# Optimization experiments

Measured on AMD Instinct MI355X. Metric: run time of the kernel, lower is better.

The kernel has to match this reference:

```python
import jax, jax.numpy as jnp
import numpy as np

DIM = 192
HEADS = 6
WIN = 64  # 8*8
EPS = 1e-12


def setup_inputs() -> dict:
    key = jax.random.key(0)
    ks = jax.random.split(key, 10)
    s = 0.02
    return {
        "qx": jax.random.normal(ks[0], (8192, WIN, DIM), jnp.float32),
        "kvx": jax.random.normal(ks[1], (4096, WIN, DIM), jnp.float32),
        "pos": jax.random.normal(ks[2], (1, WIN, DIM), jnp.float32) * s,
        "Wq": jax.random.normal(ks[3], (DIM, DIM), jnp.float32) * s,
        "bq": jnp.zeros((DIM,), jnp.float32),
        "Wkv": jax.random.normal(ks[4], (2 * DIM, DIM), jnp.float32) * s,
        "bkv": jnp.zeros((2 * DIM,), jnp.float32),
        "Wp": jax.random.normal(ks[5], (DIM, DIM), jnp.float32) * s,
        "bp": jnp.zeros((DIM,), jnp.float32),
    }


def _l2norm(x):
    # F.normalize: x / max(||x||_2, eps) along last dim
    n = jnp.sqrt(jnp.sum(x * x, axis=-1, keepdims=True))
    return x / jnp.maximum(n, EPS)


def reference(qx, kvx, pos, Wq, bq, Wkv, bkv, Wp, bp):
    B_q, q_len, C = qx.shape
    B_kv, kv_len, _ = kvx.shape
    tile_num = B_q // B_kv
    kvx = jnp.tile(kvx, (tile_num, 1, 1))
    qx = qx + pos
    q = qx @ Wq.T + bq                       # [Bq, q, C]
    kv = kvx @ Wkv.T + bkv                   # [Bq, kv, 2C]
    k, v = kv[..., :C], kv[..., C:]
    hd = C // HEADS
    q = q.reshape(B_q, q_len, HEADS, hd).transpose(0, 2, 1, 3)
    k = k.reshape(B_q, kv_len, HEADS, hd).transpose(0, 2, 1, 3)
    v = v.reshape(B_q, kv_len, HEADS, hd).transpose(0, 2, 1, 3)
    scale = 1.0 / np.sqrt(C).astype(np.float32)
    attn = jnp.einsum("bhqd,bhkd->bhqk", _l2norm(q), _l2norm(k)) * scale
    attn = jax.nn.softmax(attn, axis=-1)
    x = jnp.einsum("bhqk,bhkd->bhqd", attn, v)
    x = x.transpose(0, 2, 1, 3).reshape(B_q, q_len, C)
    return x @ Wp.T + bp
```

## Files before the change

kernel.cpp:

```cpp
#include <hip/hip_runtime.h>
#include <hip/hip_bf16.h>

#define TPB   512
#define CDIM  192
#define LDA   200
#define LDK   200
#define LDVT  72
#define LDST  200
#define VTOFF 12800
#define SCALE 0.07216878364870323f
#define EPSF  1e-12f

using short8 = __attribute__((ext_vector_type(8))) short;
using f32x4  = __attribute__((ext_vector_type(4))) float;
using us4    = __attribute__((ext_vector_type(4))) unsigned short;

__device__ __forceinline__ unsigned short hc(float f) {
  __hip_bfloat16 h = __float2bfloat16(f);
  unsigned short u; __builtin_memcpy(&u, &h, 2); return u;
}
__device__ __forceinline__ unsigned pack2(float x, float y) {
  return (unsigned)hc(x) | ((unsigned)hc(y) << 16);
}
__device__ __forceinline__ uint2 packa(f32x4 a) {
  return make_uint2(pack2(a[0], a[1]), pack2(a[2], a[3]));
}
#define MFMA(a, b, c) __builtin_amdgcn_mfma_f32_16x16x32_bf16((a), (b), (c), 0, 0, 0)
#define SCHED_FENCE() __builtin_amdgcn_sched_barrier(0)

#define NWQ  36864
#define NWKV 73728
#define NWP  36864
__global__ void cvt_weights(const float* __restrict__ Wq, const float* __restrict__ Wkv,
                            const float* __restrict__ Wp, unsigned short* __restrict__ o) {
  int i = blockIdx.x * blockDim.x + threadIdx.x;
  if (i < NWQ) o[i] = hc(Wq[i]);
  else if (i < NWQ + NWKV) o[i] = hc(Wkv[i - NWQ]);
  else if (i < NWQ + NWKV + NWP) o[i] = hc(Wp[i - NWQ - NWKV]);
}

__global__ __launch_bounds__(TPB, 4) void wa_v16(
    const float* __restrict__ qx, const float* __restrict__ kvx,
    const float* __restrict__ pos,
    const float* __restrict__ bq, const float* __restrict__ bkv,
    const float* __restrict__ bp,
    const unsigned short* __restrict__ Wqb, const unsigned short* __restrict__ Wkvb,
    const unsigned short* __restrict__ Wpb,
    float* __restrict__ out, int BQ, int BKV)
{
  __shared__ __align__(16) unsigned short sA[64 * LDA];
  __shared__ __align__(16) unsigned short sU[26624];

  const int tid = threadIdx.x;
  const int wid = tid >> 6;
  const int l15 = (tid & 63) & 15;
  const int l4  = (tid & 63) >> 4;

  int g = blockIdx.x;
  int w;
  if (BQ == 2 * BKV && (BKV & 7) == 0) {
    w = ((g >> 4) << 3) + (g & 7) + (((g >> 3) & 1) ? BKV : 0);
  } else {
    w = g;
  }
  const size_t qoff  = (size_t)w * (64 * CDIM);
  const size_t kvoff = (size_t)(w % BKV) * (64 * CDIM);

  const int srcA = l15 + 32 * (l4 & 1);
  const int srcB = srcA + 16;
  const int sel  = l4 >> 1;
  auto redistC = [&](f32x4 cA, f32x4 cB) -> short8 {
    unsigned iA0 = pack2(cA[0], cA[1]), iA1 = pack2(cA[2], cA[3]);
    unsigned iB0 = pack2(cB[0], cB[1]), iB1 = pack2(cB[2], cB[3]);
    unsigned A00 = (unsigned)__shfl((int)iA0, srcA);
    unsigned A01 = (unsigned)__shfl((int)iA1, srcA);
    unsigned A10 = (unsigned)__shfl((int)iB0, srcA);
    unsigned A11 = (unsigned)__shfl((int)iB1, srcA);
    unsigned B00 = (unsigned)__shfl((int)iA0, srcB);
    unsigned B01 = (unsigned)__shfl((int)iA1, srcB);
    unsigned B10 = (unsigned)__shfl((int)iB0, srcB);
    unsigned B11 = (unsigned)__shfl((int)iB1, srcB);
    union { uint4 u; short8 s; } uu;
    uu.u.x = sel ? A10 : A00;
    uu.u.y = sel ? A11 : A01;
    uu.u.z = sel ? B10 : B00;
    uu.u.w = sel ? B11 : B01;
    return uu.s;
  };

  {
    const float4* gq = (const float4*)(qx + qoff);
    const float4* p4 = (const float4*)pos;
    #pragma unroll
    for (int t = 0; t < 6; ++t) {
      int e = tid + t * TPB, row = e / 48, c4 = e % 48;
      float4 a = gq[e], p = p4[e];
      us4 wq;
      wq.x = hc(a.x + p.x); wq.y = hc(a.y + p.y); wq.z = hc(a.z + p.z); wq.w = hc(a.w + p.w);
      *(us4*)&sA[row * LDA + c4 * 4] = wq;
    }
    const float4* gk = (const float4*)(kvx + kvoff);
    #pragma unroll
    for (int t = 0; t < 6; ++t) {
      int e = tid + t * TPB, row = e / 48, c4 = e % 48;
      float4 k = gk[e];
      us4 wk; wk.x = hc(k.x); wk.y = hc(k.y); wk.z = hc(k.z); wk.w = hc(k.w);
      *(us4*)&sU[row * LDST + c4 * 4] = wk;
    }
  }
  __syncthreads();

  auto kproj = [&](int h, short8* kres) {
    f32x4 kacc[4][2];
    #pragma unroll
    for (int mh = 0; mh < 2; ++mh) {
      float4 bk = *(const float4*)&bkv[32 * h + 16 * mh + 4 * l4];
      #pragma unroll
      for (int n = 0; n < 4; ++n) kacc[n][mh] = f32x4{bk.x, bk.y, bk.z, bk.w};
    }
    #pragma unroll
    for (int ks = 0; ks < 6; ++ks) {
      short8 act[4];
      #pragma unroll
      for (int n = 0; n < 4; ++n)
        act[n] = *(const short8*)&sU[(16 * n + l15) * LDST + ks * 32 + 8 * l4];
      #pragma unroll
      for (int mh = 0; mh < 2; ++mh) {
        short8 kw = *(const short8*)&Wkvb[(size_t)(32 * h + 16 * mh + l15) * CDIM + ks * 32 + 8 * l4];
        #pragma unroll
        for (int n = 0; n < 4; ++n) kacc[n][mh] = MFMA(kw, act[n], kacc[n][mh]);
      }
    }
    #pragma unroll
    for (int n = 0; n < 4; ++n) {
      float ss = 0.f;
      #pragma unroll
      for (int mh = 0; mh < 2; ++mh)
        #pragma unroll
        for (int r = 0; r < 4; ++r) ss += kacc[n][mh][r] * kacc[n][mh][r];
      ss += __shfl_xor(ss, 16);
      ss += __shfl_xor(ss, 32);
      float sc = 1.0f / fmaxf(sqrtf(ss), EPSF);
      #pragma unroll
      for (int mh = 0; mh < 2; ++mh)
        #pragma unroll
        for (int r = 0; r < 4; ++r) kacc[n][mh][r] *= sc;
      kres[n] = redistC(kacc[n][0], kacc[n][1]);
    }
  };
  auto vhalf = [&](int h, int nv) {
    f32x4 vacc[4];
    {
      float bv = bkv[CDIM + 32 * h + 16 * nv + l15];
      #pragma unroll
      for (int m = 0; m < 4; ++m) vacc[m] = f32x4{bv, bv, bv, bv};
    }
    #pragma unroll
    for (int ks = 0; ks < 6; ++ks) {
      short8 vw = *(const short8*)&Wkvb[(size_t)(CDIM + 32 * h + 16 * nv + l15) * CDIM + ks * 32 + 8 * l4];
      #pragma unroll
      for (int m = 0; m < 4; ++m) {
        short8 act = *(const short8*)&sU[(16 * m + l15) * LDST + ks * 32 + 8 * l4];
        vacc[m] = MFMA(act, vw, vacc[m]);
      }
    }
    #pragma unroll
    for (int m = 0; m < 4; ++m)
      *(uint2*)&sU[VTOFF + (32 * h + 16 * nv + l15) * LDVT + 16 * m + 4 * l4] = packa(vacc[m]);
  };
  auto qproj = [&](int h, short8* qres) {
    f32x4 qacc[4][2];
    #pragma unroll
    for (int mh = 0; mh < 2; ++mh) {
      float4 bk = *(const float4*)&bq[32 * h + 16 * mh + 4 * l4];
      #pragma unroll
      for (int n = 0; n < 4; ++n) qacc[n][mh] = f32x4{bk.x, bk.y, bk.z, bk.w};
    }
    #pragma unroll
    for (int ks = 0; ks < 6; ++ks) {
      short8 act[4];
      #pragma unroll
      for (int n = 0; n < 4; ++n)
        act[n] = *(const short8*)&sA[(16 * n + l15) * LDA + ks * 32 + 8 * l4];
      #pragma unroll
      for (int mh = 0; mh < 2; ++mh) {
        short8 qw = *(const short8*)&Wqb[(size_t)(32 * h + 16 * mh + l15) * CDIM + ks * 32 + 8 * l4];
        #pragma unroll
        for (int n = 0; n < 4; ++n) qacc[n][mh] = MFMA(qw, act[n], qacc[n][mh]);
      }
    }
    #pragma unroll
    for (int n = 0; n < 4; ++n) {
      float ss = 0.f;
      #pragma unroll
      for (int mh = 0; mh < 2; ++mh)
        #pragma unroll
        for (int r = 0; r < 4; ++r) ss += qacc[n][mh][r] * qacc[n][mh][r];
      ss += __shfl_xor(ss, 16);
      ss += __shfl_xor(ss, 32);
      float sc = SCALE / fmaxf(sqrtf(ss), EPSF);
      #pragma unroll
      for (int mh = 0; mh < 2; ++mh)
        #pragma unroll
        for (int r = 0; r < 4; ++r) qacc[n][mh][r] *= sc;
      qres[n] = redistC(qacc[n][0], qacc[n][1]);
    }
  };

  short8 kres[4];
  const bool hasK = (wid < 6);
  if (hasK) {
    kproj(wid, kres);
    SCHED_FENCE();
    vhalf(wid >> 1, wid & 1);
  } else {
    const int t0 = 6 + (wid - 6) * 3;
    vhalf(t0 >> 1, t0 & 1);
    SCHED_FENCE();
    vhalf((t0 + 1) >> 1, (t0 + 1) & 1);
    SCHED_FENCE();
    vhalf((t0 + 2) >> 1, (t0 + 2) & 1);
  }
  __syncthreads();

  if (hasK) {
    #pragma unroll
    for (int n = 0; n < 4; ++n)
      *(short8*)&sU[(16 * n + l15) * LDK + wid * 32 + 8 * l4] = kres[n];
  }
  SCHED_FENCE();
  short8 qres[4];
  if (wid < 6) qproj(wid, qres);
  __syncthreads();

  if (wid < 6) {
    #pragma unroll
    for (int n = 0; n < 4; ++n)
      *(short8*)&sA[(16 * n + l15) * LDA + wid * 32 + 8 * l4] = qres[n];
  }
  __syncthreads();

  {
    const int t  = wid & 3;
    const int h0 = 3 * (wid >> 2);
    #pragma unroll
    for (int i = 0; i < 3; ++i) {
      const int hh = h0 + i;
      short8 qb = *(const short8*)&sA[(16 * t + l15) * LDA + hh * 32 + 8 * l4];
      f32x4 c[4];
      #pragma unroll
      for (int n = 0; n < 4; ++n) {
        short8 ak = *(const short8*)&sU[(16 * n + l15) * LDK + hh * 32 + 8 * l4];
        f32x4 z = f32x4{0.f, 0.f, 0.f, 0.f};
        c[n] = MFMA(ak, qb, z);
      }
      float sum = 0.f;
      #pragma unroll
      for (int n = 0; n < 4; ++n)
        #pragma unroll
        for (int r = 0; r < 4; ++r) { c[n][r] = __expf(c[n][r]); sum += c[n][r]; }
      sum += __shfl_xor(sum, 16);
      sum += __shfl_xor(sum, 32);
      const float inv = 1.0f / sum;
      #pragma unroll
      for (int n = 0; n < 4; ++n)
        #pragma unroll
        for (int r = 0; r < 4; ++r) c[n][r] *= inv;
      short8 pa0 = redistC(c[0], c[1]);
      short8 pa1 = redistC(c[2], c[3]);
      f32x4 cx0 = f32x4{0.f, 0.f, 0.f, 0.f};
      f32x4 cx1 = f32x4{0.f, 0.f, 0.f, 0.f};
      {
        short8 av00 = *(const short8*)&sU[VTOFF + (hh * 32 + l15) * LDVT + 8 * l4];
        short8 av01 = *(const short8*)&sU[VTOFF + (hh * 32 + l15) * LDVT + 32 + 8 * l4];
        cx0 = MFMA(av00, pa0, cx0);
        cx0 = MFMA(av01, pa1, cx0);
        short8 av10 = *(const short8*)&sU[VTOFF + (hh * 32 + 16 + l15) * LDVT + 8 * l4];
        short8 av11 = *(const short8*)&sU[VTOFF + (hh * 32 + 16 + l15) * LDVT + 32 + 8 * l4];
        cx1 = MFMA(av10, pa0, cx1);
        cx1 = MFMA(av11, pa1, cx1);
      }
      short8 xf = redistC(cx0, cx1);
      *(short8*)&sA[(16 * t + l15) * LDA + hh * 32 + 8 * l4] = xf;
    }
  }
  __syncthreads();

  {
    {
      const int n = wid;
      f32x4 oacc[4];
      float bv = bp[n * 16 + l15];
      #pragma unroll
      for (int m = 0; m < 4; ++m) oacc[m] = f32x4{bv, bv, bv, bv};
      #pragma unroll
      for (int ks = 0; ks < 6; ++ks) {
        short8 pw = *(const short8*)&Wpb[(size_t)(n * 16 + l15) * CDIM + ks * 32 + 8 * l4];
        #pragma unroll
        for (int m = 0; m < 4; ++m) {
          short8 xa = *(const short8*)&sA[(16 * m + l15) * LDA + ks * 32 + 8 * l4];
          oacc[m] = MFMA(xa, pw, oacc[m]);
        }
      }
      #pragma unroll
      for (int m = 0; m < 4; ++m)
        #pragma unroll
        for (int r = 0; r < 4; ++r)
          out[qoff + (size_t)(16 * m + 4 * l4 + r) * CDIM + n * 16 + l15] = oacc[m][r];
    }
    SCHED_FENCE();
    if (wid < 4) {
      const int n = wid + 8;
      f32x4 oacc[4];
      float bv = bp[n * 16 + l15];
      #pragma unroll
      for (int m = 0; m < 4; ++m) oacc[m] = f32x4{bv, bv, bv, bv};
      #pragma unroll
      for (int ks = 0; ks < 6; ++ks) {
        short8 pw = *(const short8*)&Wpb[(size_t)(n * 16 + l15) * CDIM + ks * 32 + 8 * l4];
        #pragma unroll
        for (int m = 0; m < 4; ++m) {
          short8 xa = *(const short8*)&sA[(16 * m + l15) * LDA + ks * 32 + 8 * l4];
          oacc[m] = MFMA(xa, pw, oacc[m]);
        }
      }
      #pragma unroll
      for (int m = 0; m < 4; ++m)
        #pragma unroll
        for (int r = 0; r < 4; ++r)
          out[qoff + (size_t)(16 * m + 4 * l4 + r) * CDIM + n * 16 + l15] = oacc[m][r];
    }
  }
}

extern "C" void kernel_launch(void* const* d_in, const int* in_sizes, int n_in,
                              void* d_out, int out_size, void* d_ws, size_t ws_size,
                              hipStream_t stream) {
  const float* qx  = (const float*)d_in[0];
  const float* kvx = (const float*)d_in[1];
  const float* pos = (const float*)d_in[2];
  const float* Wq  = (const float*)d_in[3];
  const float* bq  = (const float*)d_in[4];
  const float* Wkv = (const float*)d_in[5];
  const float* bkv = (const float*)d_in[6];
  const float* Wp  = (const float*)d_in[7];
  const float* bp  = (const float*)d_in[8];
  float* out = (float*)d_out;
  unsigned short* wsb = (unsigned short*)d_ws;

  const int BQ  = in_sizes[0] / (64 * CDIM);
  const int BKV = in_sizes[1] / (64 * CDIM);

  const int ncvt = NWQ + NWKV + NWP;
  cvt_weights<<<(ncvt + 255) / 256, 256, 0, stream>>>(Wq, Wkv, Wp, wsb);

  wa_v16<<<BQ, TPB, 0, stream>>>(qx, kvx, pos, bq, bkv, bp,
                                 wsb, wsb + NWQ, wsb + NWQ + NWKV, out, BQ, BKV);
}
```

Measured before the change: 465.8 us.

## Fuse output projection into attention waves with split-K reduction via LDS

Each wave now keeps its attention output fragments in registers and immediately multiplies them by the Wp slice for its three heads, accumulating all 12 output column tiles. The two wave groups that cover different head halves are then reduced through shared memory before storing. This removes the write of attention output to LDS and the separate full projection pass, but holds 12 accumulators per wave, which raises register pressure. The L2-norm and softmax divisions are also replaced with hardware rsq/rcp intrinsics.

```diff
diff --git a/kernel.cpp b/kernel.cpp
--- a/kernel.cpp
+++ b/kernel.cpp
@@ -9,7 +9,6 @@
 #define LDST  200
 #define VTOFF 12800
 #define SCALE 0.07216878364870323f
-#define EPSF  1e-12f
 
 using short8 = __attribute__((ext_vector_type(8))) short;
 using f32x4  = __attribute__((ext_vector_type(4))) float;
@@ -39,7 +38,7 @@
   else if (i < NWQ + NWKV + NWP) o[i] = hc(Wp[i - NWQ - NWKV]);
 }
 
-__global__ __launch_bounds__(TPB, 4) void wa_v16(
+__global__ __launch_bounds__(TPB, 4) void wa_v17(
     const float* __restrict__ qx, const float* __restrict__ kvx,
     const float* __restrict__ pos,
     const float* __restrict__ bq, const float* __restrict__ bkv,
@@ -140,7 +139,7 @@
         for (int r = 0; r < 4; ++r) ss += kacc[n][mh][r] * kacc[n][mh][r];
       ss += __shfl_xor(ss, 16);
       ss += __shfl_xor(ss, 32);
-      float sc = 1.0f / fmaxf(sqrtf(ss), EPSF);
+      float sc = __builtin_amdgcn_rsqf(fmaxf(ss, 1e-24f));
       #pragma unroll
       for (int mh = 0; mh < 2; ++mh)
         #pragma unroll
@@ -198,7 +197,7 @@
         for (int r = 0; r < 4; ++r) ss += qacc[n][mh][r] * qacc[n][mh][r];
       ss += __shfl_xor(ss, 16);
       ss += __shfl_xor(ss, 32);
-      float sc = SCALE / fmaxf(sqrtf(ss), EPSF);
+      float sc = SCALE * __builtin_amdgcn_rsqf(fmaxf(ss, 1e-24f));
       #pragma unroll
       for (int mh = 0; mh < 2; ++mh)
         #pragma unroll
@@ -240,9 +239,12 @@
   }
   __syncthreads();
 
+  const int t  = wid & 3;
+  const int tr = wid >> 2;
+  const int h0 = 3 * tr;
+  f32x4 oacc[12];
   {
-    const int t  = wid & 3;
-    const int h0 = 3 * (wid >> 2);
+    short8 xa[3];
     #pragma unroll
     for (int i = 0; i < 3; ++i) {
       const int hh = h0 + i;
@@ -261,7 +263,7 @@
         for (int r = 0; r < 4; ++r) { c[n][r] = __expf(c[n][r]); sum += c[n][r]; }
       sum += __shfl_xor(sum, 16);
       sum += __shfl_xor(sum, 32);
-      const float inv = 1.0f / sum;
+      const float inv = __builtin_amdgcn_rcpf(sum);
       #pragma unroll
       for (int n = 0; n < 4; ++n)
         #pragma unroll
@@ -280,55 +282,41 @@
         cx1 = MFMA(av10, pa0, cx1);
         cx1 = MFMA(av11, pa1, cx1);
       }
-      short8 xf = redistC(cx0, cx1);
-      *(short8*)&sA[(16 * t + l15) * LDA + hh * 32 + 8 * l4] = xf;
-    }
+      xa[i] = redistC(cx0, cx1);
+    }
+    SCHED_FENCE();
+    #pragma unroll
+    for (int n = 0; n < 12; ++n) {
+      float bv = (tr == 0) ? bp[n * 16 + l15] : 0.f;
+      oacc[n] = f32x4{bv, bv, bv, bv};
+    }
+    #pragma unroll
+    for (int i = 0; i < 3; ++i)
+      #pragma unroll
+      for (int n = 0; n < 12; ++n) {
+        short8 pw = *(const short8*)&Wpb[(size_t)(n * 16 + l15) * CDIM + (h0 + i) * 32 + 8 * l4];
+        oacc[n] = MFMA(xa[i], pw, oacc[n]);
+      }
   }
   __syncthreads();
 
   {
-    {
-      const int n = wid;
-      f32x4 oacc[4];
-      float bv = bp[n * 16 + l15];
-      #pragma unroll
-      for (int m = 0; m < 4; ++m) oacc[m] = f32x4{bv, bv, bv, bv};
-      #pragma unroll
-      for (int ks = 0; ks < 6; ++ks) {
-        short8 pw = *(const short8*)&Wpb[(size_t)(n * 16 + l15) * CDIM + ks * 32 + 8 * l4];
-        #pragma unroll
-        for (int m = 0; m < 4; ++m) {
-          short8 xa = *(const short8*)&sA[(16 * m + l15) * LDA + ks * 32 + 8 * l4];
-          oacc[m] = MFMA(xa, pw, oacc[m]);
-        }
-      }
-      #pragma unroll
-      for (int m = 0; m < 4; ++m)
+    float* pool = (t < 2) ? (float*)sA + t * 3072 : (float*)sU + (t - 2) * 3072;
+    const int lane = tid & 63;
+    if (tr == 1) {
+      #pragma unroll
+      for (int n = 0; n < 12; ++n)
+        *(f32x4*)(pool + n * 256 + lane * 4) = oacc[n];
+    }
+    __syncthreads();
+    if (tr == 0) {
+      #pragma unroll
+      for (int n = 0; n < 12; ++n) {
+        f32x4 p = *(const f32x4*)(pool + n * 256 + lane * 4);
         #pragma unroll
         for (int r = 0; r < 4; ++r)
-          out[qoff + (size_t)(16 * m + 4 * l4 + r) * CDIM + n * 16 + l15] = oacc[m][r];
-    }
-    SCHED_FENCE();
-    if (wid < 4) {
-      const int n = wid + 8;
-      f32x4 oacc[4];
-      float bv = bp[n * 16 + l15];
-      #pragma unroll
-      for (int m = 0; m < 4; ++m) oacc[m] = f32x4{bv, bv, bv, bv};
-      #pragma unroll
-      for (int ks = 0; ks < 6; ++ks) {
-        short8 pw = *(const short8*)&Wpb[(size_t)(n * 16 + l15) * CDIM + ks * 32 + 8 * l4];
-        #pragma unroll
-        for (int m = 0; m < 4; ++m) {
-          short8 xa = *(const short8*)&sA[(16 * m + l15) * LDA + ks * 32 + 8 * l4];
-          oacc[m] = MFMA(xa, pw, oacc[m]);
-        }
-      }
-      #pragma unroll
-      for (int m = 0; m < 4; ++m)
-        #pragma unroll
-        for (int r = 0; r < 4; ++r)
-          out[qoff + (size_t)(16 * m + 4 * l4 + r) * CDIM + n * 16 + l15] = oacc[m][r];
+          out[qoff + (size_t)(16 * t + 4 * l4 + r) * CDIM + n * 16 + l15] = oacc[n][r] + p[r];
+      }
     }
   }
 }
@@ -354,6 +342,6 @@
   const int ncvt = NWQ + NWKV + NWP;
   cvt_weights<<<(ncvt + 255) / 256, 256, 0, stream>>>(Wq, Wkv, Wp, wsb);
 
-  wa_v16<<<BQ, TPB, 0, stream>>>(qx, kvx, pos, bq, bkv, bp,
+  wa_v17<<<BQ, TPB, 0, stream>>>(qx, kvx, pos, bq, bkv, bp,
                                  wsb, wsb + NWQ, wsb + NWQ + NWKV, out, BQ, BKV);
 }
```

Result: slower. 614.4 us (+31.9%).

## Compute K/V projection once per kv window and loop over tiled query windows

Applied to the files above, without the earlier changes.

The launch now uses one block per kv window instead of one per query window. Each block projects and normalises K and V once, then loops over the tile_num query windows that share that kv window, running Q projection, attention and output projection for each. This removes the duplicated K/V projection and the duplicate kvx loads. In exchange the grid is halved (4096 blocks) and each block's work is serialised, with extra barriers around each query pass.

```diff
diff --git a/kernel.cpp b/kernel.cpp
--- a/kernel.cpp
+++ b/kernel.cpp
@@ -39,14 +39,14 @@
   else if (i < NWQ + NWKV + NWP) o[i] = hc(Wp[i - NWQ - NWKV]);
 }
 
-__global__ __launch_bounds__(TPB, 4) void wa_v16(
+__global__ __launch_bounds__(TPB, 4) void wa_v18(
     const float* __restrict__ qx, const float* __restrict__ kvx,
     const float* __restrict__ pos,
     const float* __restrict__ bq, const float* __restrict__ bkv,
     const float* __restrict__ bp,
     const unsigned short* __restrict__ Wqb, const unsigned short* __restrict__ Wkvb,
     const unsigned short* __restrict__ Wpb,
-    float* __restrict__ out, int BQ, int BKV)
+    float* __restrict__ out, int BKV, int tile_num)
 {
   __shared__ __align__(16) unsigned short sA[64 * LDA];
   __shared__ __align__(16) unsigned short sU[26624];
@@ -55,16 +55,7 @@
   const int wid = tid >> 6;
   const int l15 = (tid & 63) & 15;
   const int l4  = (tid & 63) >> 4;
-
-  int g = blockIdx.x;
-  int w;
-  if (BQ == 2 * BKV && (BKV & 7) == 0) {
-    w = ((g >> 4) << 3) + (g & 7) + (((g >> 3) & 1) ? BKV : 0);
-  } else {
-    w = g;
-  }
-  const size_t qoff  = (size_t)w * (64 * CDIM);
-  const size_t kvoff = (size_t)(w % BKV) * (64 * CDIM);
+  const size_t kvoff = (size_t)blockIdx.x * (64 * CDIM);
 
   const int srcA = l15 + 32 * (l4 & 1);
   const int srcB = srcA + 16;
@@ -88,8 +79,8 @@
     return uu.s;
   };
 
-  {
-    const float4* gq = (const float4*)(qx + qoff);
+  auto stage_q = [&](size_t qo) {
+    const float4* gq = (const float4*)(qx + qo);
     const float4* p4 = (const float4*)pos;
     #pragma unroll
     for (int t = 0; t < 6; ++t) {
@@ -99,6 +90,211 @@
       wq.x = hc(a.x + p.x); wq.y = hc(a.y + p.y); wq.z = hc(a.z + p.z); wq.w = hc(a.w + p.w);
       *(us4*)&sA[row * LDA + c4 * 4] = wq;
     }
+  };
+
+  auto kproj = [&](int h, short8* kres) {
+    f32x4 kacc[4][2];
+    #pragma unroll
+    for (int mh = 0; mh < 2; ++mh) {
+      float4 bk = *(const float4*)&bkv[32 * h + 16 * mh + 4 * l4];
+      #pragma unroll
+      for (int n = 0; n < 4; ++n) kacc[n][mh] = f32x4{bk.x, bk.y, bk.z, bk.w};
+    }
+    #pragma unroll
+    for (int ks = 0; ks < 6; ++ks) {
+      short8 act[4];
+      #pragma unroll
+      for (int n = 0; n < 4; ++n)
+        act[n] = *(const short8*)&sU[(16 * n + l15) * LDST + ks * 32 + 8 * l4];
+      #pragma unroll
+      for (int mh = 0; mh < 2; ++mh) {
+        short8 kw = *(const short8*)&Wkvb[(size_t)(32 * h + 16 * mh + l15) * CDIM + ks * 32 + 8 * l4];
+        #pragma unroll
+        for (int n = 0; n < 4; ++n) kacc[n][mh] = MFMA(kw, act[n], kacc[n][mh]);
+      }
+    }
+    #pragma unroll
+    for (int n = 0; n < 4; ++n) {
+      float ss = 0.f;
+      #pragma unroll
+      for (int mh = 0; mh < 2; ++mh)
+        #pragma unroll
+        for (int r = 0; r < 4; ++r) ss += kacc[n][mh][r] * kacc[n][mh][r];
+      ss += __shfl_xor(ss, 16);
+      ss += __shfl_xor(ss, 32);
+      float sc = 1.0f / fmaxf(sqrtf(ss), EPSF);
+      #pragma unroll
+      for (int mh = 0; mh < 2; ++mh)
+        #pragma unroll
+        for (int r = 0; r < 4; ++r) kacc[n][mh][r] *= sc;
+      kres[n] = redistC(kacc[n][0], kacc[n][1]);
+    }
+  };
+  auto vhalf = [&](int h, int nv) {
+    f32x4 vacc[4];
+    {
+      float bv = bkv[CDIM + 32 * h + 16 * nv + l15];
+      #pragma unroll
+      for (int m = 0; m < 4; ++m) vacc[m] = f32x4{bv, bv, bv, bv};
+    }
+    #pragma unroll
+    for (int ks = 0; ks < 6; ++ks) {
+      short8 vw = *(const short8*)&Wkvb[(size_t)(CDIM + 32 * h + 16 * nv + l15) * CDIM + ks * 32 + 8 * l4];
+      #pragma unroll
+      for (int m = 0; m < 4; ++m) {
+        short8 act = *(const short8*)&sU[(16 * m + l15) * LDST + ks * 32 + 8 * l4];
+        vacc[m] = MFMA(act, vw, vacc[m]);
+      }
+    }
+    #pragma unroll
+    for (int m = 0; m < 4; ++m)
+      *(uint2*)&sU[VTOFF + (32 * h + 16 * nv + l15) * LDVT + 16 * m + 4 * l4] = packa(vacc[m]);
+  };
+  auto qproj = [&](int h, short8* qres) {
+    f32x4 qacc[4][2];
+    #pragma unroll
+    for (int mh = 0; mh < 2; ++mh) {
+      float4 bk = *(const float4*)&bq[32 * h + 16 * mh + 4 * l4];
+      #pragma unroll
+      for (int n = 0; n < 4; ++n) qacc[n][mh] = f32x4{bk.x, bk.y, bk.z, bk.w};
+    }
+    #pragma unroll
+    for (int ks = 0; ks < 6; ++ks) {
+      short8 act[4];
+      #pragma unroll
+      for (int n = 0; n < 4; ++n)
+        act[n] = *(const short8*)&sA[(16 * n + l15) * LDA + ks * 32 + 8 * l4];
+      #pragma unroll
+      for (int mh = 0; mh < 2; ++mh) {
+        short8 qw = *(const short8*)&Wqb[(size_t)(32 * h + 16 * mh + l15) * CDIM + ks * 32 + 8 * l4];
+        #pragma unroll
+        for (int n = 0; n < 4; ++n) qacc[n][mh] = MFMA(qw, act[n], qacc[n][mh]);
+      }
+    }
+    #pragma unroll
+    for (int n = 0; n < 4; ++n) {
+      float ss = 0.f;
+      #pragma unroll
+      for (int mh = 0; mh < 2; ++mh)
+        #pragma unroll
+        for (int r = 0; r < 4; ++r) ss += qacc[n][mh][r] * qacc[n][mh][r];
+      ss += __shfl_xor(ss, 16);
+      ss += __shfl_xor(ss, 32);
+      float sc = SCALE / fmaxf(sqrtf(ss), EPSF);
+      #pragma unroll
+      for (int mh = 0; mh < 2; ++mh)
+        #pragma unroll
+        for (int r = 0; r < 4; ++r) qacc[n][mh][r] *= sc;
+      qres[n] = redistC(qacc[n][0], qacc[n][1]);
+    }
+  };
+
+  auto window_pass = [&](size_t qoff) {
+    short8 qres[4];
+    if (wid < 6) qproj(wid, qres);
+    __syncthreads();
+    if (wid < 6) {
+      #pragma unroll
+      for (int n = 0; n < 4; ++n)
+        *(short8*)&sA[(16 * n + l15) * LDA + wid * 32 + 8 * l4] = qres[n];
+    }
+    __syncthreads();
+
+    {
+      const int t  = wid & 3;
+      const int h0 = 3 * (wid >> 2);
+      #pragma unroll
+      for (int i = 0; i < 3; ++i) {
+        const int hh = h0 + i;
+        short8 qb = *(const short8*)&sA[(16 * t + l15) * LDA + hh * 32 + 8 * l4];
+        f32x4 c[4];
+        #pragma unroll
+        for (int n = 0; n < 4; ++n) {
+          short8 ak = *(const short8*)&sU[(16 * n + l15) * LDK + hh * 32 + 8 * l4];
+          f32x4 z = f32x4{0.f, 0.f, 0.f, 0.f};
+          c[n] = MFMA(ak, qb, z);
+        }
+        float sum = 0.f;
+        #pragma unroll
+        for (int n = 0; n < 4; ++n)
+          #pragma unroll
+          for (int r = 0; r < 4; ++r) { c[n][r] = __expf(c[n][r]); sum += c[n][r]; }
+        sum += __shfl_xor(sum, 16);
+        sum += __shfl_xor(sum, 32);
+        const float inv = 1.0f / sum;
+        #pragma unroll
+        for (int n = 0; n < 4; ++n)
+          #pragma unroll
+          for (int r = 0; r < 4; ++r) c[n][r] *= inv;
+        short8 pa0 = redistC(c[0], c[1]);
+        short8 pa1 = redistC(c[2], c[3]);
+        f32x4 cx0 = f32x4{0.f, 0.f, 0.f, 0.f};
+        f32x4 cx1 = f32x4{0.f, 0.f, 0.f, 0.f};
+        {
+          short8 av00 = *(const short8*)&sU[VTOFF + (hh * 32 + l15) * LDVT + 8 * l4];
+          short8 av01 = *(const short8*)&sU[VTOFF + (hh * 32 + l15) * LDVT + 32 + 8 * l4];
+          cx0 = MFMA(av00, pa0, cx0);
+          cx0 = MFMA(av01, pa1, cx0);
+          short8 av10 = *(const short8*)&sU[VTOFF + (hh * 32 + 16 + l15) * LDVT + 8 * l4];
+          short8 av11 = *(const short8*)&sU[VTOFF + (hh * 32 + 16 + l15) * LDVT + 32 + 8 * l4];
+          cx1 = MFMA(av10, pa0, cx1);
+          cx1 = MFMA(av11, pa1, cx1);
+        }
+        short8 xf = redistC(cx0, cx1);
+        *(short8*)&sA[(16 * t + l15) * LDA + hh * 32 + 8 * l4] = xf;
+      }
+    }
+    __syncthreads();
+
+    {
+      {
+        const int n = wid;
+        f32x4 oacc[4];
+        float bv = bp[n * 16 + l15];
+        #pragma unroll
+        for (int m = 0; m < 4; ++m) oacc[m] = f32x4{bv, bv, bv, bv};
+        #pragma unroll
+        for (int ks = 0; ks < 6; ++ks) {
+          short8 pw = *(const short8*)&Wpb[(size_t)(n * 16 + l15) * CDIM + ks * 32 + 8 * l4];
+          #pragma unroll
+          for (int m = 0; m < 4; ++m) {
+            short8 xa = *(const short8*)&sA[(16 * m + l15) * LDA + ks * 32 + 8 * l4];
+            oacc[m] = MFMA(xa, pw, oacc[m]);
+          }
+        }
+        #pragma unroll
+        for (int m = 0; m < 4; ++m)
+          #pragma unroll
+          for (int r = 0; r < 4; ++r)
+            out[qoff + (size_t)(16 * m + 4 * l4 + r) * CDIM + n * 16 + l15] = oacc[m][r];
+      }
+      SCHED_FENCE();
+      if (wid < 4) {
+        const int n = wid + 8;
+        f32x4 oacc[4];
+        float bv = bp[n * 16 + l15];
+        #pragma unroll
+        for (int m = 0; m < 4; ++m) oacc[m] = f32x4{bv, bv, bv, bv};
+        #pragma unroll
+        for (int ks = 0; ks < 6; ++ks) {
+          short8 pw = *(const short8*)&Wpb[(size_t)(n * 16 + l15) * CDIM + ks * 32 + 8 * l4];
+          #pragma unroll
+          for (int m = 0; m < 4; ++m) {
+            short8 xa = *(const short8*)&sA[(16 * m + l15) * LDA + ks * 32 + 8 * l4];
+            oacc[m] = MFMA(xa, pw, oacc[m]);
+          }
+        }
+        #pragma unroll
+        for (int m = 0; m < 4; ++m)
+          #pragma unroll
+          for (int r = 0; r < 4; ++r)
+            out[qoff + (size_t)(16 * m + 4 * l4 + r) * CDIM + n * 16 + l15] = oacc[m][r];
+      }
+    }
+  };
+
+  stage_q(kvoff);
+  {
     const float4* gk = (const float4*)(kvx + kvoff);
     #pragma unroll
     for (int t = 0; t < 6; ++t) {
@@ -109,103 +305,6 @@
     }
   }
   __syncthreads();
-
-  auto kproj = [&](int h, short8* kres) {
-    f32x4 kacc[4][2];
-    #pragma unroll
-    for (int mh = 0; mh < 2; ++mh) {
-      float4 bk = *(const float4*)&bkv[32 * h + 16 * mh + 4 * l4];
-      #pragma unroll
-      for (int n = 0; n < 4; ++n) kacc[n][mh] = f32x4{bk.x, bk.y, bk.z, bk.w};
-    }
-    #pragma unroll
-    for (int ks = 0; ks < 6; ++ks) {
-      short8 act[4];
-      #pragma unroll
-      for (int n = 0; n < 4; ++n)
-        act[n] = *(const short8*)&sU[(16 * n + l15) * LDST + ks * 32 + 8 * l4];
-      #pragma unroll
-      for (int mh = 0; mh < 2; ++mh) {
-        short8 kw = *(const short8*)&Wkvb[(size_t)(32 * h + 16 * mh + l15) * CDIM + ks * 32 + 8 * l4];
-        #pragma unroll
-        for (int n = 0; n < 4; ++n) kacc[n][mh] = MFMA(kw, act[n], kacc[n][mh]);
-      }
-    }
-    #pragma unroll
-    for (int n = 0; n < 4; ++n) {
-      float ss = 0.f;
-      #pragma unroll
-      for (int mh = 0; mh < 2; ++mh)
-        #pragma unroll
-        for (int r = 0; r < 4; ++r) ss += kacc[n][mh][r] * kacc[n][mh][r];
-      ss += __shfl_xor(ss, 16);
-      ss += __shfl_xor(ss, 32);
-      float sc = 1.0f / fmaxf(sqrtf(ss), EPSF);
-      #pragma unroll
-      for (int mh = 0; mh < 2; ++mh)
-        #pragma unroll
-        for (int r = 0; r < 4; ++r) kacc[n][mh][r] *= sc;
-      kres[n] = redistC(kacc[n][0], kacc[n][1]);
-    }
-  };
-  auto vhalf = [&](int h, int nv) {
-    f32x4 vacc[4];
-    {
-      float bv = bkv[CDIM + 32 * h + 16 * nv + l15];
-      #pragma unroll
-      for (int m = 0; m < 4; ++m) vacc[m] = f32x4{bv, bv, bv, bv};
-    }
-    #pragma unroll
-    for (int ks = 0; ks < 6; ++ks) {
-      short8 vw = *(const short8*)&Wkvb[(size_t)(CDIM + 32 * h + 16 * nv + l15) * CDIM + ks * 32 + 8 * l4];
-      #pragma unroll
-      for (int m = 0; m < 4; ++m) {
-        short8 act = *(const short8*)&sU[(16 * m + l15) * LDST + ks * 32 + 8 * l4];
-        vacc[m] = MFMA(act, vw, vacc[m]);
-      }
-    }
-    #pragma unroll
-    for (int m = 0; m < 4; ++m)
-      *(uint2*)&sU[VTOFF + (32 * h + 16 * nv + l15) * LDVT + 16 * m + 4 * l4] = packa(vacc[m]);
-  };
-  auto qproj = [&](int h, short8* qres) {
-    f32x4 qacc[4][2];
-    #pragma unroll
-    for (int mh = 0; mh < 2; ++mh) {
-      float4 bk = *(const float4*)&bq[32 * h + 16 * mh + 4 * l4];
-      #pragma unroll
-      for (int n = 0; n < 4; ++n) qacc[n][mh] = f32x4{bk.x, bk.y, bk.z, bk.w};
-    }
-    #pragma unroll
-    for (int ks = 0; ks < 6; ++ks) {
-      short8 act[4];
-      #pragma unroll
-      for (int n = 0; n < 4; ++n)
-        act[n] = *(const short8*)&sA[(16 * n + l15) * LDA + ks * 32 + 8 * l4];
-      #pragma unroll
-      for (int mh = 0; mh < 2; ++mh) {
-        short8 qw = *(const short8*)&Wqb[(size_t)(32 * h + 16 * mh + l15) * CDIM + ks * 32 + 8 * l4];
-        #pragma unroll
-        for (int n = 0; n < 4; ++n) qacc[n][mh] = MFMA(qw, act[n], qacc[n][mh]);
-      }
-    }
-    #pragma unroll
-    for (int n = 0; n < 4; ++n) {
-      float ss = 0.f;
-      #pragma unroll
-      for (int mh = 0; mh < 2; ++mh)
-        #pragma unroll
-        for (int r = 0; r < 4; ++r) ss += qacc[n][mh][r] * qacc[n][mh][r];
-      ss += __shfl_xor(ss, 16);
-      ss += __shfl_xor(ss, 32);
-      float sc = SCALE / fmaxf(sqrtf(ss), EPSF);
-      #pragma unroll
-      for (int mh = 0; mh < 2; ++mh)
-        #pragma unroll
-        for (int r = 0; r < 4; ++r) qacc[n][mh][r] *= sc;
-      qres[n] = redistC(qacc[n][0], qacc[n][1]);
-    }
-  };
 
   short8 kres[4];
   const bool hasK = (wid < 6);
@@ -229,107 +328,14 @@
       *(short8*)&sU[(16 * n + l15) * LDK + wid * 32 + 8 * l4] = kres[n];
   }
   SCHED_FENCE();
-  short8 qres[4];
-  if (wid < 6) qproj(wid, qres);
-  __syncthreads();
-
-  if (wid < 6) {
-    #pragma unroll
-    for (int n = 0; n < 4; ++n)
-      *(short8*)&sA[(16 * n + l15) * LDA + wid * 32 + 8 * l4] = qres[n];
-  }
-  __syncthreads();
-
-  {
-    const int t  = wid & 3;
-    const int h0 = 3 * (wid >> 2);
-    #pragma unroll
-    for (int i = 0; i < 3; ++i) {
-      const int hh = h0 + i;
-      short8 qb = *(const short8*)&sA[(16 * t + l15) * LDA + hh * 32 + 8 * l4];
-      f32x4 c[4];
-      #pragma unroll
-      for (int n = 0; n < 4; ++n) {
-        short8 ak = *(const short8*)&sU[(16 * n + l15) * LDK + hh * 32 + 8 * l4];
-        f32x4 z = f32x4{0.f, 0.f, 0.f, 0.f};
-        c[n] = MFMA(ak, qb, z);
-      }
-      float sum = 0.f;
-      #pragma unroll
-      for (int n = 0; n < 4; ++n)
-        #pragma unroll
-        for (int r = 0; r < 4; ++r) { c[n][r] = __expf(c[n][r]); sum += c[n][r]; }
-      sum += __shfl_xor(sum, 16);
-      sum += __shfl_xor(sum, 32);
-      const float inv = 1.0f / sum;
-      #pragma unroll
-      for (int n = 0; n < 4; ++n)
-        #pragma unroll
-        for (int r = 0; r < 4; ++r) c[n][r] *= inv;
-      short8 pa0 = redistC(c[0], c[1]);
-      short8 pa1 = redistC(c[2], c[3]);
-      f32x4 cx0 = f32x4{0.f, 0.f, 0.f, 0.f};
-      f32x4 cx1 = f32x4{0.f, 0.f, 0.f, 0.f};
-      {
-        short8 av00 = *(const short8*)&sU[VTOFF + (hh * 32 + l15) * LDVT + 8 * l4];
-        short8 av01 = *(const short8*)&sU[VTOFF + (hh * 32 + l15) * LDVT + 32 + 8 * l4];
-        cx0 = MFMA(av00, pa0, cx0);
-        cx0 = MFMA(av01, pa1, cx0);
-        short8 av10 = *(const short8*)&sU[VTOFF + (hh * 32 + 16 + l15) * LDVT + 8 * l4];
-        short8 av11 = *(const short8*)&sU[VTOFF + (hh * 32 + 16 + l15) * LDVT + 32 + 8 * l4];
-        cx1 = MFMA(av10, pa0, cx1);
-        cx1 = MFMA(av11, pa1, cx1);
-      }
-      short8 xf = redistC(cx0, cx1);
-      *(short8*)&sA[(16 * t + l15) * LDA + hh * 32 + 8 * l4] = xf;
-    }
-  }
-  __syncthreads();
-
-  {
-    {
-      const int n = wid;
-      f32x4 oacc[4];
-      float bv = bp[n * 16 + l15];
-      #pragma unroll
-      for (int m = 0; m < 4; ++m) oacc[m] = f32x4{bv, bv, bv, bv};
-      #pragma unroll
-      for (int ks = 0; ks < 6; ++ks) {
-        short8 pw = *(const short8*)&Wpb[(size_t)(n * 16 + l15) * CDIM + ks * 32 + 8 * l4];
-        #pragma unroll
-        for (int m = 0; m < 4; ++m) {
-          short8 xa = *(const short8*)&sA[(16 * m + l15) * LDA + ks * 32 + 8 * l4];
-          oacc[m] = MFMA(xa, pw, oacc[m]);
-        }
-      }
-      #pragma unroll
-      for (int m = 0; m < 4; ++m)
-        #pragma unroll
-        for (int r = 0; r < 4; ++r)
-          out[qoff + (size_t)(16 * m + 4 * l4 + r) * CDIM + n * 16 + l15] = oacc[m][r];
-    }
-    SCHED_FENCE();
-    if (wid < 4) {
-      const int n = wid + 8;
-      f32x4 oacc[4];
-      float bv = bp[n * 16 + l15];
-      #pragma unroll
-      for (int m = 0; m < 4; ++m) oacc[m] = f32x4{bv, bv, bv, bv};
-      #pragma unroll
-      for (int ks = 0; ks < 6; ++ks) {
-        short8 pw = *(const short8*)&Wpb[(size_t)(n * 16 + l15) * CDIM + ks * 32 + 8 * l4];
-        #pragma unroll
-        for (int m = 0; m < 4; ++m) {
-          short8 xa = *(const short8*)&sA[(16 * m + l15) * LDA + ks * 32 + 8 * l4];
-          oacc[m] = MFMA(xa, pw, oacc[m]);
-        }
-      }
-      #pragma unroll
-      for (int m = 0; m < 4; ++m)
-        #pragma unroll
-        for (int r = 0; r < 4; ++r)
-          out[qoff + (size_t)(16 * m + 4 * l4 + r) * CDIM + n * 16 + l15] = oacc[m][r];
-    }
+  window_pass(kvoff);
+
+  for (int j = 1; j < tile_num; ++j) {
+    __syncthreads();
+    const size_t qoff = kvoff + (size_t)j * BKV * (64 * CDIM);
+    stage_q(qoff);
+    __syncthreads();
+    window_pass(qoff);
   }
 }
 
@@ -350,10 +356,11 @@
 
   const int BQ  = in_sizes[0] / (64 * CDIM);
   const int BKV = in_sizes[1] / (64 * CDIM);
+  const int tile_num = BQ / BKV;
 
   const int ncvt = NWQ + NWKV + NWP;
   cvt_weights<<<(ncvt + 255) / 256, 256, 0, stream>>>(Wq, Wkv, Wp, wsb);
 
-  wa_v16<<<BQ, TPB, 0, stream>>>(qx, kvx, pos, bq, bkv, bp,
-                                 wsb, wsb + NWQ, wsb + NWQ + NWKV, out, BQ, BKV);
-}
+  wa_v18<<<BKV, TPB, 0, stream>>>(qx, kvx, pos, bq, bkv, bp,
+                                  wsb, wsb + NWQ, wsb + NWQ + NWKV, out, BKV, tile_num);
+}
```

Measured after the change: 527.1 us. 13.2% more time.
